# Kernel optimization log

Hardware: AMD Instinct MI355X
Metric: run time of the kernel (lower is better)

The kernel has to match this reference:

```python
import jax, jax.numpy as jnp
import numpy as np

B, LQ, H, NH, LK, N = 32, 256, 256, 8, 512, 8192
DH = H // NH
EPS = 1e-12

def layer_norm(x, g, b):
    m = x.mean(-1, keepdims=True)
    v = ((x - m) ** 2).mean(-1, keepdims=True)
    return (x - m) / jnp.sqrt(v + EPS) * g + b

def setup_inputs() -> dict:
    rs = np.random.RandomState(0)
    counts = rs.randint(LK // 2, LK + 1, size=B)  # ragged per-graph edge counts, max = LK
    E = int(counts.sum())
    edge_batch = jnp.asarray(np.repeat(np.arange(B), counts), jnp.int32)
    edge_pos = jnp.asarray(np.concatenate([np.arange(c) for c in counts]), jnp.int32)
    pad_mask = jnp.asarray((np.arange(LK)[None, :] < counts[:, None]).astype(np.float32))
    src = jnp.asarray(rs.randint(0, N, E), jnp.int32)
    dst = jnp.asarray(rs.randint(0, N, E), jnp.int32)
    ks = jax.random.split(jax.random.key(0), 16)
    def rn(i, shape, s=0.02):
        return jax.random.normal(ks[i], shape, jnp.float32) * s
    return dict(
        extended_attention_mask=jnp.zeros((B, 1, 1, LQ), jnp.float32),
        query=rn(0, (B, LQ, H), 1.0),
        rel_embedding_output=rn(1, (E, H), 1.0),
        graph_output=rn(2, (N, H), 1.0),
        src=src, dst=dst, edge_batch=edge_batch, edge_pos=edge_pos, pad_mask=pad_mask,
        Wq=rn(3, (H, H)), bq=jnp.zeros((H,), jnp.float32),
        Wk=rn(4, (2 * H, H)), bk=jnp.zeros((H,), jnp.float32),
        Wv=rn(5, (H, H)), bv=jnp.zeros((H,), jnp.float32),
        Wo=rn(6, (H, H)), bo=jnp.zeros((H,), jnp.float32),
        ln1_g=jnp.ones((H,), jnp.float32), ln1_b=jnp.zeros((H,), jnp.float32),
        W1=rn(7, (H, H)), b1=jnp.zeros((H,), jnp.float32),
        W2=rn(8, (H, H)), b2=jnp.zeros((H,), jnp.float32),
        ln2_g=jnp.ones((H,), jnp.float32), ln2_b=jnp.zeros((H,), jnp.float32),
    )

def reference(extended_attention_mask, query, rel_embedding_output, graph_output,
              src, dst, edge_batch, edge_pos, pad_mask,
              Wq, bq, Wk, bk, Wv, bv, Wo, bo, ln1_g, ln1_b,
              W1, b1, W2, b2, ln2_g, ln2_b):
    # --- memory_transform: edge gather + ragged pad (vectorized scatter) ---
    key_flat = jnp.concatenate([graph_output[src], rel_embedding_output], -1)  # [E, 2H]
    dst_flat = graph_output[dst]                                               # [E, H]
    key_pad = jnp.zeros((B, LK, 2 * H), key_flat.dtype).at[edge_batch, edge_pos].set(key_flat)
    val_pad = jnp.zeros((B, LK, H), dst_flat.dtype).at[edge_batch, edge_pos].set(dst_flat)
    cross_mask = (1.0 - pad_mask)[:, None, None, :] * -10000.0                 # [B,1,1,LK]
    # --- BidiAttention ---
    Q = (query @ Wq + bq).reshape(B, LQ, NH, DH)
    K = (key_pad @ Wk + bk).reshape(B, LK, NH, DH)
    V = (val_pad @ Wv + bv).reshape(B, LK, NH, DH)
    scores = jnp.einsum('bqhd,bkhd->bhqk', Q, K) / np.float32(np.sqrt(DH))
    pq = jax.nn.softmax(scores + cross_mask, axis=-1)
    query_ctx = jnp.einsum('bhqk,bkhd->bqhd', pq, V).reshape(B, LQ, H)
    pv = jax.nn.softmax(scores.transpose(0, 1, 3, 2) + extended_attention_mask, axis=-1)
    value_ctx = jnp.einsum('bhkq,bqhd->bkhd', pv, Q).reshape(B, LK, H)
    # --- RelAwareCross output / gate ---
    query_out = layer_norm(query_ctx @ Wo + bo + query, ln1_g, ln1_b)
    theta = jax.nn.sigmoid(value_ctx @ W1 + b1 + val_pad @ W2 + b2)
    value_new = layer_norm(theta * value_ctx + (1.0 - theta) * val_pad, ln2_g, ln2_b)
    # --- memory_update: unpad + scatter-mean by dst, replace rows with incoming edges ---
    val_edges = value_new[edge_batch, edge_pos]                                # [E, H]
    sums = jax.ops.segment_sum(val_edges, dst, num_segments=N)
    cnts = jax.ops.segment_sum(jnp.ones((val_edges.shape[0],), val_edges.dtype), dst, num_segments=N)
    mean = sums / jnp.maximum(cnts, 1.0)[:, None]
    graph_new = jnp.where((cnts > 0)[:, None], mean, graph_output)
    return (graph_new, query_out)
```

## Files before the change

kernel.cpp:

```cpp
#include <hip/hip_runtime.h>
#include <hip/hip_bf16.h>
#include <string.h>

#define B_ 32
#define LQ_ 256
#define H_ 256
#define NH_ 8
#define LK_ 512
#define N_ 8192
#define DH_ 32

typedef float floatx4 __attribute__((ext_vector_type(4)));
typedef short shortx8 __attribute__((ext_vector_type(8)));

__device__ __forceinline__ short f2b(float f) {
    __hip_bfloat16 h = __float2bfloat16(f);
    short s;
    __builtin_memcpy(&s, &h, 2);
    return s;
}
__device__ __forceinline__ float b2f(short s) {
    unsigned u = ((unsigned)(unsigned short)s) << 16;
    float f;
    __builtin_memcpy(&f, &u, 4);
    return f;
}

__global__ __launch_bounds__(256) void phase1(
    const float* __restrict__ graph, const float* __restrict__ rel,
    const int* __restrict__ src, const int* __restrict__ dst,
    const int* __restrict__ eb, const float* __restrict__ pad_mask,
    const float* __restrict__ Wq, const float* __restrict__ Wk,
    const float* __restrict__ Wv, const float* __restrict__ Wo,
    const float* __restrict__ W1, const float* __restrict__ W2,
    short* __restrict__ WT, short* __restrict__ key_pad,
    short* __restrict__ val_pad, float* __restrict__ zbase, int E) {
    const int bid = blockIdx.x, tid = threadIdx.x;
    if (bid < 8192) {
        int row = bid * 2 + (tid >> 7);
        int t = tid & 127;
        int b = row >> 9, p = row & 511;
        bool valid = pad_mask[row] > 0.5f;
        size_t krow = (size_t)row * 512;
        size_t vrow = (size_t)row * 256;
        int kc = t * 4, vc = t * 2;
        if (valid) {
            int lo = 0, hi = E;
            while (lo < hi) { int mid = (lo + hi) >> 1; if (eb[mid] < b) lo = mid + 1; else hi = mid; }
            int e = lo + p;
            int s = src[e], d = dst[e];
            const float* sp = (kc < 256) ? (graph + (size_t)s * 256 + kc)
                                         : (rel + (size_t)e * 256 + (kc - 256));
            float4 k4 = *(const float4*)sp;
            key_pad[krow + kc + 0] = f2b(k4.x);
            key_pad[krow + kc + 1] = f2b(k4.y);
            key_pad[krow + kc + 2] = f2b(k4.z);
            key_pad[krow + kc + 3] = f2b(k4.w);
            float2 v2 = *(const float2*)(graph + (size_t)d * 256 + vc);
            val_pad[vrow + vc + 0] = f2b(v2.x);
            val_pad[vrow + vc + 1] = f2b(v2.y);
        } else {
            *(long long*)&key_pad[krow + kc] = 0;
            *(int*)&val_pad[vrow + vc] = 0;
        }
    } else if (bid < 9984) {
        int i = (bid - 8192) * 256 + tid;
        const float* s;
        int K, loc;
        if (i < 65536) { s = Wq; K = 256; loc = i; }
        else if (i < 196608) { s = Wk; K = 512; loc = i - 65536; }
        else {
            int m = (i - 196608) >> 16;
            loc = (i - 196608) & 65535;
            K = 256;
            s = (m == 0) ? Wv : (m == 1) ? Wo : (m == 2) ? W1 : W2;
        }
        int n = loc / K, k = loc - n * K;
        WT[i] = f2b(s[(size_t)k * 256 + n]);
    } else {
        long long n = (long long)N_ * H_ + N_;
        for (long long i = (long long)(bid - 9984) * 256 + tid; i < n; i += 512 * 256)
            zbase[i] = 0.f;
    }
}

__global__ __launch_bounds__(256) void phase2_gemm(
    const float* __restrict__ query, const short* __restrict__ key_pad,
    const short* __restrict__ val_pad, const short* __restrict__ WT,
    const float* __restrict__ bq, const float* __restrict__ bk,
    const float* __restrict__ bv,
    short* __restrict__ Qb, short* __restrict__ Kb, short* __restrict__ Vb) {
    __shared__ short As[64][40];
    __shared__ short Bs[64][40];
    const int tid = threadIdx.x;
    const int id = blockIdx.x;
    const float* Af = nullptr;
    const short* Ab = nullptr;
    const short* WTp;
    const float* bias;
    short* C;
    int K, rb, cb;
    if (id < 512) { rb = id >> 2; cb = id & 3; Af = query; K = 256; WTp = WT; bias = bq; C = Qb; }
    else if (id < 1536) { int t = id - 512; rb = t >> 2; cb = t & 3; Ab = key_pad; K = 512; WTp = WT + 65536; bias = bk; C = Kb; }
    else { int t = id - 1536; rb = t >> 2; cb = t & 3; Ab = val_pad; K = 256; WTp = WT + 196608; bias = bv; C = Vb; }
    const int row0 = rb * 64, col0 = cb * 64;
    const int wv = tid >> 6, lane = tid & 63;
    const int mw = (wv & 1) * 32, nw = (wv >> 1) * 32;
    const int lm = lane & 15, quad = lane >> 4;

    floatx4 acc[2][2] = {{{0.f, 0.f, 0.f, 0.f}, {0.f, 0.f, 0.f, 0.f}},
                         {{0.f, 0.f, 0.f, 0.f}, {0.f, 0.f, 0.f, 0.f}}};

    for (int kc = 0; kc < K; kc += 32) {
        {
            int r = tid >> 2, kq = (tid & 3) * 8;
            if (Af) {
                const float* ap = Af + (size_t)(row0 + r) * K + kc + kq;
                float4 a1 = *(const float4*)ap, a2 = *(const float4*)(ap + 4);
                As[r][kq + 0] = f2b(a1.x); As[r][kq + 1] = f2b(a1.y);
                As[r][kq + 2] = f2b(a1.z); As[r][kq + 3] = f2b(a1.w);
                As[r][kq + 4] = f2b(a2.x); As[r][kq + 5] = f2b(a2.y);
                As[r][kq + 6] = f2b(a2.z); As[r][kq + 7] = f2b(a2.w);
            } else {
                *(shortx8*)&As[r][kq] =
                    *(const shortx8*)(Ab + (size_t)(row0 + r) * K + kc + kq);
            }
        }
        {
            int n = tid >> 2, kq = (tid & 3) * 8;
            *(shortx8*)&Bs[n][kq] =
                *(const shortx8*)(WTp + (size_t)(col0 + n) * K + kc + kq);
        }
        __syncthreads();
        shortx8 a0 = *(const shortx8*)&As[mw + lm][quad * 8];
        shortx8 a1 = *(const shortx8*)&As[mw + 16 + lm][quad * 8];
        shortx8 b0 = *(const shortx8*)&Bs[nw + lm][quad * 8];
        shortx8 b1 = *(const shortx8*)&Bs[nw + 16 + lm][quad * 8];
        acc[0][0] = __builtin_amdgcn_mfma_f32_16x16x32_bf16(a0, b0, acc[0][0], 0, 0, 0);
        acc[0][1] = __builtin_amdgcn_mfma_f32_16x16x32_bf16(a0, b1, acc[0][1], 0, 0, 0);
        acc[1][0] = __builtin_amdgcn_mfma_f32_16x16x32_bf16(a1, b0, acc[1][0], 0, 0, 0);
        acc[1][1] = __builtin_amdgcn_mfma_f32_16x16x32_bf16(a1, b1, acc[1][1], 0, 0, 0);
        __syncthreads();
    }
#pragma unroll
    for (int i = 0; i < 2; i++) {
#pragma unroll
        for (int j = 0; j < 2; j++) {
            int gn = col0 + nw + j * 16 + lm;
            float bvv = bias[gn];
#pragma unroll
            for (int r = 0; r < 4; r++) {
                int gm = row0 + mw + i * 16 + quad * 4 + r;
                C[(size_t)gm * 256 + gn] = f2b(acc[i][j][r] + bvv);
            }
        }
    }
}

__global__ __launch_bounds__(256) void phase3_attn(
    const short* __restrict__ Qm, const short* __restrict__ Km,
    const short* __restrict__ Vm, const float* __restrict__ pad_mask,
    const float* __restrict__ ext, short* __restrict__ qctx,
    short* __restrict__ vctx) {
    __shared__ short SB1[64][40];
    __shared__ short SB2[128][40];
    __shared__ short SB3[32][136];
    __shared__ short SB4[64][136];
    __shared__ float rowinv[64];
    const int tid = threadIdx.x;
    const int wv = tid >> 6, lane = tid & 63;
    const int lm = lane & 15, quad = lane >> 4;
    const float scale = 0.17677669529663687f;
    const int id = blockIdx.x;

    if (id < 1024) {
        const int q0 = (id & 3) * 64, h = (id >> 2) & 7, b = id >> 5;
        {
            int r = tid >> 2, dq = (tid & 3) * 8;
            *(shortx8*)&SB1[r][dq] =
                *(const shortx8*)(Qm + ((size_t)(b * LQ_ + q0 + r)) * H_ + h * DH_ + dq);
        }
        floatx4 oacc0 = {0.f, 0.f, 0.f, 0.f}, oacc1 = {0.f, 0.f, 0.f, 0.f};
        float psum[4] = {0.f, 0.f, 0.f, 0.f};
        shortx8 aq;
        for (int c = 0; c < 4; c++) {
            const int kbase = c * 128;
            {
                int r = tid >> 1, dq = (tid & 1) * 16;
                const short* kp = Km + ((size_t)(b * LK_ + kbase + r)) * H_ + h * DH_ + dq;
                *(shortx8*)&SB2[r][dq] = *(const shortx8*)kp;
                *(shortx8*)&SB2[r][dq + 8] = *(const shortx8*)(kp + 8);
                const short* vp = Vm + ((size_t)(b * LK_ + kbase + r)) * H_ + h * DH_ + dq;
                shortx8 v1 = *(const shortx8*)vp;
                shortx8 v2 = *(const shortx8*)(vp + 8);
#pragma unroll
                for (int i = 0; i < 8; i++) {
                    SB3[dq + i][r] = v1[i];
                    SB3[dq + 8 + i][r] = v2[i];
                }
            }
            __syncthreads();
            if (c == 0) aq = *(const shortx8*)&SB1[wv * 16 + lm][quad * 8];
#pragma unroll
            for (int nt = 0; nt < 8; nt++) {
                shortx8 bk = *(const shortx8*)&SB2[nt * 16 + lm][quad * 8];
                floatx4 s = {0.f, 0.f, 0.f, 0.f};
                s = __builtin_amdgcn_mfma_f32_16x16x32_bf16(aq, bk, s, 0, 0, 0);
                float mk = (1.0f - pad_mask[b * LK_ + kbase + nt * 16 + lm]) * -10000.0f;
#pragma unroll
                for (int r = 0; r < 4; r++) {
                    float e = __expf(s[r] * scale + mk);
                    psum[r] += e;
                    SB4[wv * 16 + quad * 4 + r][nt * 16 + lm] = f2b(e);
                }
            }
            __syncthreads();
#pragma unroll
            for (int kk = 0; kk < 4; kk++) {
                shortx8 pa = *(const shortx8*)&SB4[wv * 16 + lm][kk * 32 + quad * 8];
                shortx8 b0 = *(const shortx8*)&SB3[lm][kk * 32 + quad * 8];
                shortx8 b1 = *(const shortx8*)&SB3[16 + lm][kk * 32 + quad * 8];
                oacc0 = __builtin_amdgcn_mfma_f32_16x16x32_bf16(pa, b0, oacc0, 0, 0, 0);
                oacc1 = __builtin_amdgcn_mfma_f32_16x16x32_bf16(pa, b1, oacc1, 0, 0, 0);
            }
            __syncthreads();
        }
#pragma unroll
        for (int r = 0; r < 4; r++) {
            float s2 = psum[r];
            s2 += __shfl_down(s2, 8, 64);
            s2 += __shfl_down(s2, 4, 64);
            s2 += __shfl_down(s2, 2, 64);
            s2 += __shfl_down(s2, 1, 64);
            if (lm == 0) rowinv[wv * 16 + quad * 4 + r] = 1.0f / s2;
        }
        __syncthreads();
#pragma unroll
        for (int r = 0; r < 4; r++) {
            float inv = rowinv[wv * 16 + quad * 4 + r];
            int q = q0 + wv * 16 + quad * 4 + r;
            short* op = qctx + ((size_t)(b * LQ_ + q)) * H_ + h * DH_;
            op[lm] = f2b(oacc0[r] * inv);
            op[16 + lm] = f2b(oacc1[r] * inv);
        }
    } else {
        const int id2 = id - 1024;
        const int k0 = (id2 & 7) * 64, h = (id2 >> 3) & 7, b = id2 >> 6;
        {
            int r = tid >> 2, dq = (tid & 3) * 8;
            *(shortx8*)&SB1[r][dq] =
                *(const shortx8*)(Km + ((size_t)(b * LK_ + k0 + r)) * H_ + h * DH_ + dq);
        }
        floatx4 oacc0 = {0.f, 0.f, 0.f, 0.f}, oacc1 = {0.f, 0.f, 0.f, 0.f};
        float psum[4] = {0.f, 0.f, 0.f, 0.f};
        shortx8 ak;
        for (int c = 0; c < 2; c++) {
            const int qbase = c * 128;
            {
                int r = tid >> 1, dq = (tid & 1) * 16;
                const short* qp = Qm + ((size_t)(b * LQ_ + qbase + r)) * H_ + h * DH_ + dq;
                shortx8 q1 = *(const shortx8*)qp;
                shortx8 q2 = *(const shortx8*)(qp + 8);
                *(shortx8*)&SB2[r][dq] = q1;
                *(shortx8*)&SB2[r][dq + 8] = q2;
#pragma unroll
                for (int i = 0; i < 8; i++) {
                    SB3[dq + i][r] = q1[i];
                    SB3[dq + 8 + i][r] = q2[i];
                }
            }
            __syncthreads();
            if (c == 0) ak = *(const shortx8*)&SB1[wv * 16 + lm][quad * 8];
#pragma unroll
            for (int nt = 0; nt < 8; nt++) {
                shortx8 bq = *(const shortx8*)&SB2[nt * 16 + lm][quad * 8];
                floatx4 s = {0.f, 0.f, 0.f, 0.f};
                s = __builtin_amdgcn_mfma_f32_16x16x32_bf16(ak, bq, s, 0, 0, 0);
                float mk = ext[b * LQ_ + qbase + nt * 16 + lm];
#pragma unroll
                for (int r = 0; r < 4; r++) {
                    float e = __expf(s[r] * scale + mk);
                    psum[r] += e;
                    SB4[wv * 16 + quad * 4 + r][nt * 16 + lm] = f2b(e);
                }
            }
            __syncthreads();
#pragma unroll
            for (int kk = 0; kk < 4; kk++) {
                shortx8 pa = *(const shortx8*)&SB4[wv * 16 + lm][kk * 32 + quad * 8];
                shortx8 b0 = *(const shortx8*)&SB3[lm][kk * 32 + quad * 8];
                shortx8 b1 = *(const shortx8*)&SB3[16 + lm][kk * 32 + quad * 8];
                oacc0 = __builtin_amdgcn_mfma_f32_16x16x32_bf16(pa, b0, oacc0, 0, 0, 0);
                oacc1 = __builtin_amdgcn_mfma_f32_16x16x32_bf16(pa, b1, oacc1, 0, 0, 0);
            }
            __syncthreads();
        }
#pragma unroll
        for (int r = 0; r < 4; r++) {
            float s2 = psum[r];
            s2 += __shfl_down(s2, 8, 64);
            s2 += __shfl_down(s2, 4, 64);
            s2 += __shfl_down(s2, 2, 64);
            s2 += __shfl_down(s2, 1, 64);
            if (lm == 0) rowinv[wv * 16 + quad * 4 + r] = 1.0f / s2;
        }
        __syncthreads();
#pragma unroll
        for (int r = 0; r < 4; r++) {
            float inv = rowinv[wv * 16 + quad * 4 + r];
            int k = k0 + wv * 16 + quad * 4 + r;
            short* op = vctx + ((size_t)(b * LK_ + k)) * H_ + h * DH_;
            op[lm] = f2b(oacc0[r] * inv);
            op[16 + lm] = f2b(oacc1[r] * inv);
        }
    }
}

__global__ __launch_bounds__(256) void phase4_tail(
    const short* __restrict__ qctx, const short* __restrict__ WTo,
    const float* __restrict__ bo, const float* __restrict__ query,
    const float* __restrict__ g1, const float* __restrict__ be1,
    float* __restrict__ out_q,
    const short* __restrict__ vctx, const short* __restrict__ val_pad,
    const short* __restrict__ WT1, const short* __restrict__ WT2,
    const float* __restrict__ b1_, const float* __restrict__ b2_,
    const float* __restrict__ g2, const float* __restrict__ be2,
    const float* __restrict__ pad_mask, const int* __restrict__ eb,
    const int* __restrict__ dst, float* __restrict__ sums,
    int* __restrict__ icnts, int E) {
    __shared__ short As1[64][40];
    __shared__ short As2[64][40];
    __shared__ short Bs1[256][40];
    __shared__ short Bs2[256][40];
    const int tid = threadIdx.x;
    const int wv = tid >> 6, lane = tid & 63;
    const int lm = lane & 15, quad = lane >> 4;
    floatx4 acc[16];
#pragma unroll
    for (int i = 0; i < 16; i++) acc[i] = (floatx4){0.f, 0.f, 0.f, 0.f};

    if (blockIdx.x < 128) {
        const int row0 = blockIdx.x * 64;
        for (int kc = 0; kc < 256; kc += 32) {
            {
                int r = tid >> 2, kq = (tid & 3) * 8;
                *(shortx8*)&As1[r][kq] =
                    *(const shortx8*)(qctx + (size_t)(row0 + r) * 256 + kc + kq);
            }
#pragma unroll
            for (int j = 0; j < 4; j++)
                *(shortx8*)&Bs1[tid][j * 8] =
                    *(const shortx8*)(WTo + (size_t)tid * 256 + kc + j * 8);
            __syncthreads();
            shortx8 a = *(const shortx8*)&As1[wv * 16 + lm][quad * 8];
#pragma unroll
            for (int nt = 0; nt < 16; nt++) {
                shortx8 bf = *(const shortx8*)&Bs1[nt * 16 + lm][quad * 8];
                acc[nt] = __builtin_amdgcn_mfma_f32_16x16x32_bf16(a, bf, acc[nt], 0, 0, 0);
            }
            __syncthreads();
        }
#pragma unroll
        for (int r = 0; r < 4; r++) {
            int gm = row0 + wv * 16 + quad * 4 + r;
            float x[16];
            float ssum = 0.f;
#pragma unroll
            for (int nt = 0; nt < 16; nt++) {
                int gn = nt * 16 + lm;
                x[nt] = acc[nt][r] + bo[gn] + query[(size_t)gm * 256 + gn];
                ssum += x[nt];
            }
            ssum += __shfl_down(ssum, 8, 64);
            ssum += __shfl_down(ssum, 4, 64);
            ssum += __shfl_down(ssum, 2, 64);
            ssum += __shfl_down(ssum, 1, 64);
            ssum = __shfl(ssum, lane & 48, 64);
            float mean = ssum * (1.0f / 256.0f);
            float vsum = 0.f;
#pragma unroll
            for (int nt = 0; nt < 16; nt++) {
                float dv = x[nt] - mean;
                x[nt] = dv;
                vsum += dv * dv;
            }
            vsum += __shfl_down(vsum, 8, 64);
            vsum += __shfl_down(vsum, 4, 64);
            vsum += __shfl_down(vsum, 2, 64);
            vsum += __shfl_down(vsum, 1, 64);
            vsum = __shfl(vsum, lane & 48, 64);
            float rstd = rsqrtf(vsum * (1.0f / 256.0f) + 1e-12f);
#pragma unroll
            for (int nt = 0; nt < 16; nt++) {
                int gn = nt * 16 + lm;
                out_q[(size_t)gm * 256 + gn] = x[nt] * rstd * g1[gn] + be1[gn];
            }
        }
    } else {
        const int row0 = (blockIdx.x - 128) * 64;
        for (int kc = 0; kc < 256; kc += 32) {
            {
                int r = tid >> 2, kq = (tid & 3) * 8;
                *(shortx8*)&As1[r][kq] =
                    *(const shortx8*)(vctx + (size_t)(row0 + r) * 256 + kc + kq);
                *(shortx8*)&As2[r][kq] =
                    *(const shortx8*)(val_pad + (size_t)(row0 + r) * 256 + kc + kq);
            }
#pragma unroll
            for (int j = 0; j < 4; j++) {
                *(shortx8*)&Bs1[tid][j * 8] =
                    *(const shortx8*)(WT1 + (size_t)tid * 256 + kc + j * 8);
                *(shortx8*)&Bs2[tid][j * 8] =
                    *(const shortx8*)(WT2 + (size_t)tid * 256 + kc + j * 8);
            }
            __syncthreads();
            shortx8 a1 = *(const shortx8*)&As1[wv * 16 + lm][quad * 8];
            shortx8 a2 = *(const shortx8*)&As2[wv * 16 + lm][quad * 8];
#pragma unroll
            for (int nt = 0; nt < 16; nt++) {
                shortx8 bf1 = *(const shortx8*)&Bs1[nt * 16 + lm][quad * 8];
                shortx8 bf2 = *(const shortx8*)&Bs2[nt * 16 + lm][quad * 8];
                acc[nt] = __builtin_amdgcn_mfma_f32_16x16x32_bf16(a1, bf1, acc[nt], 0, 0, 0);
                acc[nt] = __builtin_amdgcn_mfma_f32_16x16x32_bf16(a2, bf2, acc[nt], 0, 0, 0);
            }
            __syncthreads();
        }
        int b = row0 >> 9;
        int lo = 0, hi = E;
        while (lo < hi) { int mid = (lo + hi) >> 1; if (eb[mid] < b) lo = mid + 1; else hi = mid; }
#pragma unroll
        for (int r = 0; r < 4; r++) {
            int gm = row0 + wv * 16 + quad * 4 + r;
            float x[16];
            float ssum = 0.f;
#pragma unroll
            for (int nt = 0; nt < 16; nt++) {
                int gn = nt * 16 + lm;
                float t = acc[nt][r] + b1_[gn] + b2_[gn];
                float th = 1.0f / (1.0f + __expf(-t));
                float vc = b2f(vctx[(size_t)gm * 256 + gn]);
                float vp = b2f(val_pad[(size_t)gm * 256 + gn]);
                x[nt] = th * vc + (1.0f - th) * vp;
                ssum += x[nt];
            }
            ssum += __shfl_down(ssum, 8, 64);
            ssum += __shfl_down(ssum, 4, 64);
            ssum += __shfl_down(ssum, 2, 64);
            ssum += __shfl_down(ssum, 1, 64);
            ssum = __shfl(ssum, lane & 48, 64);
            float mean = ssum * (1.0f / 256.0f);
            float vsum = 0.f;
#pragma unroll
            for (int nt = 0; nt < 16; nt++) {
                float dv = x[nt] - mean;
                x[nt] = dv;
                vsum += dv * dv;
            }
            vsum += __shfl_down(vsum, 8, 64);
            vsum += __shfl_down(vsum, 4, 64);
            vsum += __shfl_down(vsum, 2, 64);
            vsum += __shfl_down(vsum, 1, 64);
            vsum = __shfl(vsum, lane & 48, 64);
            float rstd = rsqrtf(vsum * (1.0f / 256.0f) + 1e-12f);
            if (!(pad_mask[gm] > 0.5f)) continue;
            int d = dst[lo + (gm & 511)];
#pragma unroll
            for (int nt = 0; nt < 16; nt++) {
                int gn = nt * 16 + lm;
                atomicAdd(&sums[(size_t)d * 256 + gn], x[nt] * rstd * g2[gn] + be2[gn]);
            }
            if (lm == 0) atomicAdd(&icnts[d], 1);
        }
    }
}

__global__ __launch_bounds__(256) void finalize_graph(
    const float* __restrict__ sums, const int* __restrict__ icnts,
    const float* __restrict__ graph, float* __restrict__ out_g) {
    int n = blockIdx.x, c = threadIdx.x;
    long long idx = (long long)n * H_ + c;
    int cnt = icnts[n];
    out_g[idx] = (cnt > 0) ? sums[idx] / (float)cnt : graph[idx];
}

extern "C" void kernel_launch(void* const* d_in, const int* in_sizes, int n_in,
                              void* d_out, int out_size, void* d_ws, size_t ws_size,
                              hipStream_t stream) {
    const float* ext_mask = (const float*)d_in[0];
    const float* query    = (const float*)d_in[1];
    const float* rel      = (const float*)d_in[2];
    const float* graph    = (const float*)d_in[3];
    const int*  src      = (const int*)d_in[4];
    const int*  dst      = (const int*)d_in[5];
    const int*  eb       = (const int*)d_in[6];
    const int*  ep       = (const int*)d_in[7];
    const float* pad_mask = (const float*)d_in[8];
    const float* Wq = (const float*)d_in[9];  const float* bq = (const float*)d_in[10];
    const float* Wk = (const float*)d_in[11]; const float* bk = (const float*)d_in[12];
    const float* Wv = (const float*)d_in[13]; const float* bv = (const float*)d_in[14];
    const float* Wo = (const float*)d_in[15]; const float* bo = (const float*)d_in[16];
    const float* g1 = (const float*)d_in[17]; const float* be1 = (const float*)d_in[18];
    const float* W1 = (const float*)d_in[19]; const float* b1 = (const float*)d_in[20];
    const float* W2 = (const float*)d_in[21]; const float* b2 = (const float*)d_in[22];
    const float* g2 = (const float*)d_in[23]; const float* be2 = (const float*)d_in[24];
    const int E = in_sizes[2] / H_;

    float* out_g = (float*)d_out;
    float* out_q = (float*)d_out + (size_t)N_ * H_;

    short* sp = (short*)d_ws;
    short* key_pad = sp; sp += (size_t)B_ * LK_ * 2 * H_;
    short* val_pad = sp; sp += (size_t)B_ * LK_ * H_;
    short* Qb      = sp; sp += (size_t)B_ * LQ_ * H_;
    short* Kb      = sp; sp += (size_t)B_ * LK_ * H_;
    short* Vb      = sp; sp += (size_t)B_ * LK_ * H_;
    short* qctx    = sp; sp += (size_t)B_ * LQ_ * H_;
    short* vctx    = sp; sp += (size_t)B_ * LK_ * H_;
    short* WT      = sp; sp += 458752;
    short* WTo = WT + 262144;
    short* WT1 = WT + 327680;
    short* WT2 = WT + 393216;
    float* fp = (float*)(((size_t)sp + 15) & ~(size_t)15);
    float* sums = fp; fp += (size_t)N_ * H_;
    int*   icnts = (int*)fp;

    phase1<<<10496, 256, 0, stream>>>(graph, rel, src, dst, eb, pad_mask,
                                      Wq, Wk, Wv, Wo, W1, W2,
                                      WT, key_pad, val_pad, sums, E);
    phase2_gemm<<<2560, 256, 0, stream>>>(query, key_pad, val_pad, WT,
                                          bq, bk, bv, Qb, Kb, Vb);
    phase3_attn<<<3072, 256, 0, stream>>>(Qb, Kb, Vb, pad_mask, ext_mask,
                                          qctx, vctx);
    phase4_tail<<<384, 256, 0, stream>>>(qctx, WTo, bo, query, g1, be1, out_q,
                                         vctx, val_pad, WT1, WT2, b1, b2, g2, be2,
                                         pad_mask, eb, dst, sums, icnts, E);
    finalize_graph<<<N_, 256, 0, stream>>>(sums, icnts, graph, out_g);
}
```

Measured before the change: 280.3 us.

## Split fused tail GEMM+layernorm into tiled GEMM and per-row layernorm kernels

The fused phase4 kernel ran only 384 blocks, each computing a full 64x256 output row tile plus layernorm and the scatter atomics. It is replaced by a 64x64-tiled GEMM kernel with 1536 blocks that writes fp32 results to workspace buffers, followed by a per-row layernorm/gate/scatter kernel with one block per row. The aim is to fill the GPU better, since the old launch left many CUs underused. In exchange it writes and rereads about 24 MB of fp32 intermediates, adds a kernel launch, and runs the binary search once per row instead of once per block.

```diff
diff --git a/kernel.cpp b/kernel.cpp
--- a/kernel.cpp
+++ b/kernel.cpp
@@ -316,161 +316,134 @@
     }
 }
 
-__global__ __launch_bounds__(256) void phase4_tail(
-    const short* __restrict__ qctx, const short* __restrict__ WTo,
-    const float* __restrict__ bo, const float* __restrict__ query,
-    const float* __restrict__ g1, const float* __restrict__ be1,
-    float* __restrict__ out_q,
-    const short* __restrict__ vctx, const short* __restrict__ val_pad,
+__global__ __launch_bounds__(256) void phase4a_gemm(
+    const short* __restrict__ qctx, const short* __restrict__ vctx,
+    const short* __restrict__ val_pad, const short* __restrict__ WTo,
     const short* __restrict__ WT1, const short* __restrict__ WT2,
-    const float* __restrict__ b1_, const float* __restrict__ b2_,
-    const float* __restrict__ g2, const float* __restrict__ be2,
-    const float* __restrict__ pad_mask, const int* __restrict__ eb,
-    const int* __restrict__ dst, float* __restrict__ sums,
-    int* __restrict__ icnts, int E) {
+    float* __restrict__ obuf, float* __restrict__ tbuf) {
     __shared__ short As1[64][40];
     __shared__ short As2[64][40];
-    __shared__ short Bs1[256][40];
-    __shared__ short Bs2[256][40];
+    __shared__ short Bs1[64][40];
+    __shared__ short Bs2[64][40];
     const int tid = threadIdx.x;
+    const int id = blockIdx.x;
+    const bool is_out = id < 512;
+    int t = is_out ? id : id - 512;
+    const int row0 = (t >> 2) * 64, col0 = (t & 3) * 64;
     const int wv = tid >> 6, lane = tid & 63;
+    const int mw = (wv & 1) * 32, nw = (wv >> 1) * 32;
     const int lm = lane & 15, quad = lane >> 4;
-    floatx4 acc[16];
-#pragma unroll
-    for (int i = 0; i < 16; i++) acc[i] = (floatx4){0.f, 0.f, 0.f, 0.f};
-
-    if (blockIdx.x < 128) {
-        const int row0 = blockIdx.x * 64;
-        for (int kc = 0; kc < 256; kc += 32) {
-            {
-                int r = tid >> 2, kq = (tid & 3) * 8;
-                *(shortx8*)&As1[r][kq] =
-                    *(const shortx8*)(qctx + (size_t)(row0 + r) * 256 + kc + kq);
-            }
-#pragma unroll
-            for (int j = 0; j < 4; j++)
-                *(shortx8*)&Bs1[tid][j * 8] =
-                    *(const shortx8*)(WTo + (size_t)tid * 256 + kc + j * 8);
-            __syncthreads();
-            shortx8 a = *(const shortx8*)&As1[wv * 16 + lm][quad * 8];
-#pragma unroll
-            for (int nt = 0; nt < 16; nt++) {
-                shortx8 bf = *(const shortx8*)&Bs1[nt * 16 + lm][quad * 8];
-                acc[nt] = __builtin_amdgcn_mfma_f32_16x16x32_bf16(a, bf, acc[nt], 0, 0, 0);
-            }
-            __syncthreads();
-        }
-#pragma unroll
-        for (int r = 0; r < 4; r++) {
-            int gm = row0 + wv * 16 + quad * 4 + r;
-            float x[16];
-            float ssum = 0.f;
-#pragma unroll
-            for (int nt = 0; nt < 16; nt++) {
-                int gn = nt * 16 + lm;
-                x[nt] = acc[nt][r] + bo[gn] + query[(size_t)gm * 256 + gn];
-                ssum += x[nt];
-            }
-            ssum += __shfl_down(ssum, 8, 64);
-            ssum += __shfl_down(ssum, 4, 64);
-            ssum += __shfl_down(ssum, 2, 64);
-            ssum += __shfl_down(ssum, 1, 64);
-            ssum = __shfl(ssum, lane & 48, 64);
-            float mean = ssum * (1.0f / 256.0f);
-            float vsum = 0.f;
-#pragma unroll
-            for (int nt = 0; nt < 16; nt++) {
-                float dv = x[nt] - mean;
-                x[nt] = dv;
-                vsum += dv * dv;
-            }
-            vsum += __shfl_down(vsum, 8, 64);
-            vsum += __shfl_down(vsum, 4, 64);
-            vsum += __shfl_down(vsum, 2, 64);
-            vsum += __shfl_down(vsum, 1, 64);
-            vsum = __shfl(vsum, lane & 48, 64);
-            float rstd = rsqrtf(vsum * (1.0f / 256.0f) + 1e-12f);
-#pragma unroll
-            for (int nt = 0; nt < 16; nt++) {
-                int gn = nt * 16 + lm;
-                out_q[(size_t)gm * 256 + gn] = x[nt] * rstd * g1[gn] + be1[gn];
-            }
-        }
+
+    floatx4 acc[2][2] = {{{0.f, 0.f, 0.f, 0.f}, {0.f, 0.f, 0.f, 0.f}},
+                         {{0.f, 0.f, 0.f, 0.f}, {0.f, 0.f, 0.f, 0.f}}};
+
+    for (int kc = 0; kc < 256; kc += 32) {
+        int r = tid >> 2, kq = (tid & 3) * 8;
+        if (is_out) {
+            *(shortx8*)&As1[r][kq] =
+                *(const shortx8*)(qctx + (size_t)(row0 + r) * 256 + kc + kq);
+            *(shortx8*)&Bs1[r][kq] =
+                *(const shortx8*)(WTo + (size_t)(col0 + r) * 256 + kc + kq);
+        } else {
+            *(shortx8*)&As1[r][kq] =
+                *(const shortx8*)(vctx + (size_t)(row0 + r) * 256 + kc + kq);
+            *(shortx8*)&As2[r][kq] =
+                *(const shortx8*)(val_pad + (size_t)(row0 + r) * 256 + kc + kq);
+            *(shortx8*)&Bs1[r][kq] =
+                *(const shortx8*)(WT1 + (size_t)(col0 + r) * 256 + kc + kq);
+            *(shortx8*)&Bs2[r][kq] =
+                *(const shortx8*)(WT2 + (size_t)(col0 + r) * 256 + kc + kq);
+        }
+        __syncthreads();
+        shortx8 a0 = *(const shortx8*)&As1[mw + lm][quad * 8];
+        shortx8 a1 = *(const shortx8*)&As1[mw + 16 + lm][quad * 8];
+        shortx8 b0 = *(const shortx8*)&Bs1[nw + lm][quad * 8];
+        shortx8 b1 = *(const shortx8*)&Bs1[nw + 16 + lm][quad * 8];
+        acc[0][0] = __builtin_amdgcn_mfma_f32_16x16x32_bf16(a0, b0, acc[0][0], 0, 0, 0);
+        acc[0][1] = __builtin_amdgcn_mfma_f32_16x16x32_bf16(a0, b1, acc[0][1], 0, 0, 0);
+        acc[1][0] = __builtin_amdgcn_mfma_f32_16x16x32_bf16(a1, b0, acc[1][0], 0, 0, 0);
+        acc[1][1] = __builtin_amdgcn_mfma_f32_16x16x32_bf16(a1, b1, acc[1][1], 0, 0, 0);
+        if (!is_out) {
+            shortx8 c0 = *(const shortx8*)&As2[mw + lm][quad * 8];
+            shortx8 c1 = *(const shortx8*)&As2[mw + 16 + lm][quad * 8];
+            shortx8 d0 = *(const shortx8*)&Bs2[nw + lm][quad * 8];
+            shortx8 d1 = *(const shortx8*)&Bs2[nw + 16 + lm][quad * 8];
+            acc[0][0] = __builtin_amdgcn_mfma_f32_16x16x32_bf16(c0, d0, acc[0][0], 0, 0, 0);
+            acc[0][1] = __builtin_amdgcn_mfma_f32_16x16x32_bf16(c0, d1, acc[0][1], 0, 0, 0);
+            acc[1][0] = __builtin_amdgcn_mfma_f32_16x16x32_bf16(c1, d0, acc[1][0], 0, 0, 0);
+            acc[1][1] = __builtin_amdgcn_mfma_f32_16x16x32_bf16(c1, d1, acc[1][1], 0, 0, 0);
+        }
+        __syncthreads();
+    }
+    float* C = is_out ? obuf : tbuf;
+#pragma unroll
+    for (int i = 0; i < 2; i++) {
+#pragma unroll
+        for (int j = 0; j < 2; j++) {
+            int gn = col0 + nw + j * 16 + lm;
+#pragma unroll
+            for (int r = 0; r < 4; r++) {
+                int gm = row0 + mw + i * 16 + quad * 4 + r;
+                C[(size_t)gm * 256 + gn] = acc[i][j][r];
+            }
+        }
+    }
+}
+
+__global__ __launch_bounds__(256) void phase4b_ln(
+    const float* __restrict__ obuf, const float* __restrict__ bo,
+    const float* __restrict__ query, const float* __restrict__ g1,
+    const float* __restrict__ be1, float* __restrict__ out_q,
+    const float* __restrict__ tbuf, const short* __restrict__ vctx,
+    const short* __restrict__ val_pad, const float* __restrict__ b1_,
+    const float* __restrict__ b2_, const float* __restrict__ g2,
+    const float* __restrict__ be2, const float* __restrict__ pad_mask,
+    const int* __restrict__ eb, const int* __restrict__ dst,
+    float* __restrict__ sums, int* __restrict__ icnts, int E) {
+    __shared__ float red[8];
+    const int c = threadIdx.x;
+    const int wave = c >> 6;
+    if (blockIdx.x < 8192) {
+        int row = blockIdx.x;
+        long long idx = (long long)row * H_ + c;
+        float x = obuf[idx] + bo[c] + query[idx];
+        float t = x;
+        for (int off = 32; off > 0; off >>= 1) t += __shfl_down(t, off, 64);
+        if ((c & 63) == 0) red[wave] = t;
+        __syncthreads();
+        float mean = (red[0] + red[1] + red[2] + red[3]) * (1.0f / H_);
+        float dv = x - mean;
+        float v = dv * dv;
+        for (int off = 32; off > 0; off >>= 1) v += __shfl_down(v, off, 64);
+        if ((c & 63) == 0) red[4 + wave] = v;
+        __syncthreads();
+        float var = (red[4] + red[5] + red[6] + red[7]) * (1.0f / H_);
+        out_q[idx] = dv * rsqrtf(var + 1e-12f) * g1[c] + be1[c];
     } else {
-        const int row0 = (blockIdx.x - 128) * 64;
-        for (int kc = 0; kc < 256; kc += 32) {
-            {
-                int r = tid >> 2, kq = (tid & 3) * 8;
-                *(shortx8*)&As1[r][kq] =
-                    *(const shortx8*)(vctx + (size_t)(row0 + r) * 256 + kc + kq);
-                *(shortx8*)&As2[r][kq] =
-                    *(const shortx8*)(val_pad + (size_t)(row0 + r) * 256 + kc + kq);
-            }
-#pragma unroll
-            for (int j = 0; j < 4; j++) {
-                *(shortx8*)&Bs1[tid][j * 8] =
-                    *(const shortx8*)(WT1 + (size_t)tid * 256 + kc + j * 8);
-                *(shortx8*)&Bs2[tid][j * 8] =
-                    *(const shortx8*)(WT2 + (size_t)tid * 256 + kc + j * 8);
-            }
-            __syncthreads();
-            shortx8 a1 = *(const shortx8*)&As1[wv * 16 + lm][quad * 8];
-            shortx8 a2 = *(const shortx8*)&As2[wv * 16 + lm][quad * 8];
-#pragma unroll
-            for (int nt = 0; nt < 16; nt++) {
-                shortx8 bf1 = *(const shortx8*)&Bs1[nt * 16 + lm][quad * 8];
-                shortx8 bf2 = *(const shortx8*)&Bs2[nt * 16 + lm][quad * 8];
-                acc[nt] = __builtin_amdgcn_mfma_f32_16x16x32_bf16(a1, bf1, acc[nt], 0, 0, 0);
-                acc[nt] = __builtin_amdgcn_mfma_f32_16x16x32_bf16(a2, bf2, acc[nt], 0, 0, 0);
-            }
-            __syncthreads();
-        }
-        int b = row0 >> 9;
+        int row = blockIdx.x - 8192;
+        bool valid = pad_mask[row] > 0.5f;
+        if (!valid) return;
+        long long idx = (long long)row * H_ + c;
+        float th = 1.0f / (1.0f + __expf(-(tbuf[idx] + b1_[c] + b2_[c])));
+        float x = th * b2f(vctx[idx]) + (1.0f - th) * b2f(val_pad[idx]);
+        float t = x;
+        for (int off = 32; off > 0; off >>= 1) t += __shfl_down(t, off, 64);
+        if ((c & 63) == 0) red[wave] = t;
+        __syncthreads();
+        float mean = (red[0] + red[1] + red[2] + red[3]) * (1.0f / H_);
+        float dv = x - mean;
+        float v = dv * dv;
+        for (int off = 32; off > 0; off >>= 1) v += __shfl_down(v, off, 64);
+        if ((c & 63) == 0) red[4 + wave] = v;
+        __syncthreads();
+        float var = (red[4] + red[5] + red[6] + red[7]) * (1.0f / H_);
+        float y = dv * rsqrtf(var + 1e-12f) * g2[c] + be2[c];
+        int b = row >> 9;
         int lo = 0, hi = E;
         while (lo < hi) { int mid = (lo + hi) >> 1; if (eb[mid] < b) lo = mid + 1; else hi = mid; }
-#pragma unroll
-        for (int r = 0; r < 4; r++) {
-            int gm = row0 + wv * 16 + quad * 4 + r;
-            float x[16];
-            float ssum = 0.f;
-#pragma unroll
-            for (int nt = 0; nt < 16; nt++) {
-                int gn = nt * 16 + lm;
-                float t = acc[nt][r] + b1_[gn] + b2_[gn];
-                float th = 1.0f / (1.0f + __expf(-t));
-                float vc = b2f(vctx[(size_t)gm * 256 + gn]);
-                float vp = b2f(val_pad[(size_t)gm * 256 + gn]);
-                x[nt] = th * vc + (1.0f - th) * vp;
-                ssum += x[nt];
-            }
-            ssum += __shfl_down(ssum, 8, 64);
-            ssum += __shfl_down(ssum, 4, 64);
-            ssum += __shfl_down(ssum, 2, 64);
-            ssum += __shfl_down(ssum, 1, 64);
-            ssum = __shfl(ssum, lane & 48, 64);
-            float mean = ssum * (1.0f / 256.0f);
-            float vsum = 0.f;
-#pragma unroll
-            for (int nt = 0; nt < 16; nt++) {
-                float dv = x[nt] - mean;
-                x[nt] = dv;
-                vsum += dv * dv;
-            }
-            vsum += __shfl_down(vsum, 8, 64);
-            vsum += __shfl_down(vsum, 4, 64);
-            vsum += __shfl_down(vsum, 2, 64);
-            vsum += __shfl_down(vsum, 1, 64);
-            vsum = __shfl(vsum, lane & 48, 64);
-            float rstd = rsqrtf(vsum * (1.0f / 256.0f) + 1e-12f);
-            if (!(pad_mask[gm] > 0.5f)) continue;
-            int d = dst[lo + (gm & 511)];
-#pragma unroll
-            for (int nt = 0; nt < 16; nt++) {
-                int gn = nt * 16 + lm;
-                atomicAdd(&sums[(size_t)d * 256 + gn], x[nt] * rstd * g2[gn] + be2[gn]);
-            }
-            if (lm == 0) atomicAdd(&icnts[d], 1);
-        }
+        int d = dst[lo + (row & 511)];
+        atomicAdd(&sums[(size_t)d * 256 + c], y);
+        if (c == 0) atomicAdd(&icnts[d], 1);
     }
 }
 
@@ -522,7 +495,9 @@
     short* WT2 = WT + 393216;
     float* fp = (float*)(((size_t)sp + 15) & ~(size_t)15);
     float* sums = fp; fp += (size_t)N_ * H_;
-    int*   icnts = (int*)fp;
+    int*   icnts = (int*)fp; fp += N_;
+    float* obuf = fp; fp += (size_t)B_ * LQ_ * H_;
+    float* tbuf = fp; fp += (size_t)B_ * LK_ * H_;
 
     phase1<<<10496, 256, 0, stream>>>(graph, rel, src, dst, eb, pad_mask,
                                       Wq, Wk, Wv, Wo, W1, W2,
@@ -531,8 +506,10 @@
                                           bq, bk, bv, Qb, Kb, Vb);
     phase3_attn<<<3072, 256, 0, stream>>>(Qb, Kb, Vb, pad_mask, ext_mask,
                                           qctx, vctx);
-    phase4_tail<<<384, 256, 0, stream>>>(qctx, WTo, bo, query, g1, be1, out_q,
-                                         vctx, val_pad, WT1, WT2, b1, b2, g2, be2,
-                                         pad_mask, eb, dst, sums, icnts, E);
+    phase4a_gemm<<<1536, 256, 0, stream>>>(qctx, vctx, val_pad, WTo, WT1, WT2,
+                                           obuf, tbuf);
+    phase4b_ln<<<24576, 256, 0, stream>>>(obuf, bo, query, g1, be1, out_q,
+                                          tbuf, vctx, val_pad, b1, b2, g2, be2,
+                                          pad_mask, eb, dst, sums, icnts, E);
     finalize_graph<<<N_, 256, 0, stream>>>(sums, icnts, graph, out_g);
 }
```

After: 273.7 us. -2.4%, faster.
